# Performance work log

Hardware: AMD Instinct MI355X
Metric: run time of the kernel (lower is better)

The kernel has to match this reference:

```python
import jax, jax.numpy as jnp
import numpy as np

N, D, K = 16384, 256, 4096  # encoded vectors, embedding_dim, codebook_size


def setup_inputs() -> dict:
    key = jax.random.key(0)
    k_ze, k_cb = jax.random.split(key)
    ze = jax.random.normal(k_ze, (N, D), dtype=jnp.float32)
    codebook = jax.random.normal(k_cb, (K, D), dtype=jnp.float32)
    return {"ze": ze, "codebook": codebook}


def reference(ze, codebook):
    # Pairwise squared distances: ||ze||^2 + ||e||^2 - 2 ze e^T  -> [N, K]
    sq_norm = (
        jnp.sum(ze ** 2, axis=-1, keepdims=True)
        + jnp.sum(codebook ** 2, axis=1)
        - 2.0 * jnp.matmul(ze, codebook.T)
    )
    indices = jnp.argmin(sq_norm, axis=-1)            # [N]
    zq = jnp.take(codebook, indices, axis=0)          # [N, D] gather

    # VQ losses (stop-gradient mirrors .detach())
    vq_e_loss = jnp.mean((zq - jax.lax.stop_gradient(ze)) ** 2)
    vq_commit_loss = jnp.mean((jax.lax.stop_gradient(zq) - ze) ** 2)

    # perplexity: probs[i] = count_i / 10 (faithful to original, incl. /10)
    counts = jnp.zeros((K,), dtype=jnp.float32).at[indices].add(1.0)
    probs = counts / 10.0
    perplexity = jnp.exp(-jnp.sum(probs * jnp.log(probs + 1e-10)))

    return indices, zq, vq_e_loss, vq_commit_loss, perplexity
```

## Files before the change

kernel.cpp:

```cpp
#include <hip/hip_runtime.h>
#include <math.h>

#define N_TOT 16384
#define DIM   256
#define KCB   4096

typedef __attribute__((ext_vector_type(8)))  short s8v;
typedef __attribute__((ext_vector_type(16))) float f16v;

#define PK_OFF   32832
#define CBF_OFF  163904
#define WS_NEED  4358208ull
#define ZERO_W   36880

__device__ __forceinline__ void gload16(const void* g, void* l) {
  __builtin_amdgcn_global_load_lds(
      (const __attribute__((address_space(1))) unsigned int*)g,
      (__attribute__((address_space(3))) unsigned int*)l, 16, 0, 0);
}

__global__ __launch_bounds__(256)
void cb_prep_k(const float* __restrict__ cb, float* __restrict__ ws) {
  __shared__ float Cf[32 * 260];
  const int t = threadIdx.x, tile = blockIdx.x;
  for (int i = tile * 256 + t; i < ZERO_W; i += 128 * 256) ws[KCB + i] = 0.0f;

  const int c0 = tile * 32;
  {
    int r = t >> 3, q = t & 7;
    const float4* src4 = (const float4*)(cb + (size_t)(c0 + r) * DIM);
    float4* dst = (float4*)&Cf[r * 260];
    #pragma unroll
    for (int i = 0; i < 8; ++i) dst[q + 8 * i] = src4[q + 8 * i];
  }
  __syncthreads();

  const int col = t >> 3, j = t & 7;
  ushort* tb = (ushort*)((char*)ws + CBF_OFF) + (size_t)tile * 16384;
  const float* rowp = Cf + col * 260;
  float s = 0.0f;
  #pragma unroll
  for (int ks = 0; ks < 16; ++ks) {
    #pragma unroll
    for (int kh = 0; kh < 2; ++kh) {
      float x = rowp[ks * 16 + kh * 8 + j];
      s += x * x;
      unsigned xb = __float_as_uint(x);
      unsigned hb = xb & 0xFFFF0000u;
      float lf = x - __uint_as_float(hb);
      tb[ks * 512 + kh * 256 + t]        = (ushort)(xb >> 16);
      tb[8192 + ks * 512 + kh * 256 + t] = (ushort)(__float_as_uint(lf) >> 16);
    }
  }
  s += __shfl_down(s, 4, 8);
  s += __shfl_down(s, 2, 8);
  s += __shfl_down(s, 1, 8);
  if (j == 0) ws[c0 + col] = s;
}

__global__ __launch_bounds__(256, 2)
void vq_mfma_k(const float* __restrict__ ze, float* __restrict__ ws) {
  __shared__ __align__(16) char ldsU[66560];

  const int t    = threadIdx.x;
  const int lane = t & 63;
  const int w    = t >> 6;
  const int ln31 = lane & 31;
  const int hl   = lane >> 5;
  const int cq   = blockIdx.x >> 7;
  const int mb   = blockIdx.x & 127;
  const int m0   = mb * 128;

  const float* cbn = ws;
  unsigned long long* pk = (unsigned long long*)((char*)ws + PK_OFF);
  const char* cbF = (const char*)ws + CBF_OFF;

  s8v ah[16], al[16];
  float* Af = (float*)ldsU;
  #pragma unroll 1
  for (int ph = 0; ph < 2; ++ph) {
    __syncthreads();
    {
      int r = t >> 2, q = t & 3;
      const float4* src4 = (const float4*)(ze + (size_t)(m0 + ph * 64 + r) * DIM);
      float4* dst = (float4*)&Af[r * 260];
      #pragma unroll
      for (int i = 0; i < 16; ++i) dst[q + 4 * i] = src4[q + 4 * i];
    }
    __syncthreads();
    if ((w >> 1) == ph) {
      int rl = (w & 1) * 32 + ln31;
      const float* rowp = Af + rl * 260;
      #pragma unroll
      for (int ks = 0; ks < 16; ++ks) {
        float4 x0 = *(const float4*)(rowp + ks * 16 + hl * 8);
        float4 x1 = *(const float4*)(rowp + ks * 16 + hl * 8 + 4);
        float xs[8] = {x0.x, x0.y, x0.z, x0.w, x1.x, x1.y, x1.z, x1.w};
        #pragma unroll
        for (int j = 0; j < 8; ++j) {
          unsigned xb = __float_as_uint(xs[j]);
          unsigned hb = xb & 0xFFFF0000u;
          float lf = xs[j] - __uint_as_float(hb);
          ah[ks][j] = (short)(xb >> 16);
          al[ks][j] = (short)(__float_as_uint(lf) >> 16);
        }
      }
    }
  }
  __syncthreads();

  char* bufs0 = ldsU;
  char* bufs1 = ldsU + 32768;
  const char* qbase = cbF + (size_t)cq * 32 * 32768;

  {
    const char* g = qbase + (size_t)w * 1024 + (size_t)(lane & 63) * 16;
    char* lp = bufs0 + w * 1024 + (lane & 63) * 0;
    #pragma unroll
    for (int ii = 0; ii < 8; ++ii) gload16(g + ii * 4096, bufs0 + w * 1024 + ii * 4096);
    (void)lp;
  }

  float cvn = cbn[cq * 1024 + ln31];

  float best[16];
  int   bidx[16];
  #pragma unroll
  for (int r = 0; r < 16; ++r) { best[r] = -1e30f; bidx[r] = 0; }

  #pragma unroll 1
  for (int tt = 0; tt < 32; ++tt) {
    __syncthreads();
    if (tt + 1 < 32) {
      const char* g = qbase + (size_t)(tt + 1) * 32768 + (size_t)w * 1024 + (size_t)lane * 16;
      char* lp = ((tt + 1) & 1 ? bufs1 : bufs0) + w * 1024;
      #pragma unroll
      for (int ii = 0; ii < 8; ++ii) gload16(g + ii * 4096, lp + ii * 4096);
    }

    const float half_cv = 0.5f * cvn;
    if (tt + 1 < 32) cvn = cbn[cq * 1024 + (tt + 1) * 32 + ln31];
    const char* bc = (tt & 1) ? bufs1 : bufs0;

    f16v hh, xx;
    #pragma unroll
    for (int r = 0; r < 16; ++r) { hh[r] = 0.0f; xx[r] = 0.0f; }

    #pragma unroll
    for (int ks = 0; ks < 16; ++ks) {
      s8v bh = *(const s8v*)(bc + ks * 1024 + lane * 16);
      s8v bl = *(const s8v*)(bc + 16384 + ks * 1024 + lane * 16);
      hh = __builtin_amdgcn_mfma_f32_32x32x16_bf16(ah[ks], bh, hh, 0, 0, 0);
      xx = __builtin_amdgcn_mfma_f32_32x32x16_bf16(ah[ks], bl, xx, 0, 0, 0);
      xx = __builtin_amdgcn_mfma_f32_32x32x16_bf16(al[ks], bh, xx, 0, 0, 0);
    }

    const int c0 = cq * 1024 + tt * 32 + ln31;
    #pragma unroll
    for (int r = 0; r < 16; ++r) {
      float s = hh[r] + xx[r] - half_cv;
      if (s > best[r]) { best[r] = s; bidx[r] = c0; }
    }
  }

  #pragma unroll
  for (int r = 0; r < 16; ++r) {
    float s = best[r];
    int   c = bidx[r];
    #pragma unroll
    for (int mk = 1; mk < 32; mk <<= 1) {
      float os = __shfl_xor(s, mk, 64);
      int   oc = __shfl_xor(c, mk, 64);
      if (os > s || (os == s && oc < c)) { s = os; c = oc; }
    }
    if (ln31 == 0) {
      int row = m0 + w * 32 + (r & 3) + 8 * (r >> 2) + 4 * hl;
      unsigned u = __float_as_uint(s);
      unsigned enc = (u & 0x80000000u) ? ~u : (u | 0x80000000u);
      unsigned long long p = ((unsigned long long)enc << 32) | (unsigned)(KCB - 1 - c);
      atomicMax(&pk[row], p);
    }
  }
}

__global__ __launch_bounds__(256)
void gather_k(const float* __restrict__ ze, const float* __restrict__ cb,
              float* __restrict__ ws, float* __restrict__ out) {
  __shared__ int sIdx[32];
  const int t  = threadIdx.x;
  const int m0 = blockIdx.x * 32;
  float* counts   = ws + KCB;
  float* loss_sum = ws + 2 * KCB;
  const unsigned long long* pk = (const unsigned long long*)((const char*)ws + PK_OFF);

  if (t < 32) {
    unsigned long long p = pk[m0 + t];
    int col = KCB - 1 - (int)(unsigned)(p & 0xFFFFFFFFull);
    out[m0 + t] = (float)col;
    sIdx[t] = col;
    atomicAdd(&counts[col], 1.0f);
  }
  __syncthreads();

  float* out_zq = out + N_TOT;
  const int w = t >> 6, ln = t & 63;
  float lsum = 0.0f;
  #pragma unroll
  for (int p = 0; p < 8; ++p) {
    int r = w + 4 * p;
    float4 cvv = *(const float4*)(cb + (size_t)sIdx[r] * DIM + ln * 4);
    float4 zv  = *(const float4*)(ze + (size_t)(m0 + r) * DIM + ln * 4);
    *(float4*)(out_zq + (size_t)(m0 + r) * DIM + ln * 4) = cvv;
    float dx = cvv.x - zv.x, dy = cvv.y - zv.y, dz = cvv.z - zv.z, dw = cvv.w - zv.w;
    lsum += dx * dx + dy * dy + dz * dz + dw * dw;
  }
  #pragma unroll
  for (int off = 32; off > 0; off >>= 1) lsum += __shfl_down(lsum, off, 64);
  if (ln == 0) atomicAdd(loss_sum, lsum);
}

__global__ void zero_ws_k(float* __restrict__ ws, int nw) {
  int i = blockIdx.x * 256 + threadIdx.x;
  if (i < nw) ws[KCB + i] = 0.0f;
}

__global__ void cbnorm_k(const float* __restrict__ cb, float* __restrict__ ws) {
  int row  = blockIdx.x * 4 + (threadIdx.x >> 6);
  int lane = threadIdx.x & 63;
  float4 v = *(const float4*)(cb + (size_t)row * DIM + lane * 4);
  float s = v.x*v.x + v.y*v.y + v.z*v.z + v.w*v.w;
  #pragma unroll
  for (int off = 32; off > 0; off >>= 1) s += __shfl_down(s, off, 64);
  if (lane == 0) ws[row] = s;
}

#define FBM 32
#define FBN 64
#define FBD 128
__global__ __launch_bounds__(256, 4)
void vq_main_k(const float* __restrict__ ze, const float* __restrict__ cb,
               float* __restrict__ ws, float* __restrict__ out) {
  __shared__ float As[FBM * FBD];
  __shared__ float Bs[FBN * FBD];
  __shared__ float red_d[FBM * 16];
  __shared__ int   red_i[FBM * 16];
  __shared__ int   sIdx[FBM];

  const int t  = threadIdx.x;
  const int tx = t & 15;
  const int ty = t >> 4;
  const int m0 = blockIdx.x * FBM;

  const float* cbn = ws;
  float* counts    = ws + KCB;
  float* loss_sum  = ws + 2 * KCB;

  float best0 = 1e30f, best1 = 1e30f;
  int   bidx0 = 0,     bidx1 = 0;
  const int sA = ty & 7;
  const int sB = tx & 7;

  for (int kt = 0; kt < KCB / FBN; ++kt) {
    float cbnj[4];
    #pragma unroll
    for (int j = 0; j < 4; ++j) cbnj[j] = cbn[kt * FBN + tx + 16 * j];
    float acc[2][4];
    #pragma unroll
    for (int i = 0; i < 2; ++i)
      #pragma unroll
      for (int j = 0; j < 4; ++j) acc[i][j] = 0.0f;

    for (int dc = 0; dc < DIM / FBD; ++dc) {
      __syncthreads();
      {
        int c  = t & 31;
        int rb = t >> 5;
        #pragma unroll
        for (int p = 0; p < 4; ++p) {
          int r = rb + 8 * p;
          float4 v = *(const float4*)(ze + (size_t)(m0 + r) * DIM + dc * FBD + c * 4);
          *(float4*)&As[r * FBD + ((c ^ (r & 7)) << 2)] = v;
        }
        #pragma unroll
        for (int p = 0; p < 8; ++p) {
          int r = rb + 8 * p;
          float4 v = *(const float4*)(cb + (size_t)(kt * FBN + r) * DIM + dc * FBD + c * 4);
          *(float4*)&Bs[r * FBD + ((c ^ (r & 7)) << 2)] = v;
        }
      }
      __syncthreads();
      #pragma unroll 8
      for (int ds = 0; ds < FBD / 4; ++ds) {
        float4 a0 = *(const float4*)&As[ty * FBD + ((ds ^ sA) << 2)];
        float4 a1 = *(const float4*)&As[(ty + 16) * FBD + ((ds ^ sA) << 2)];
        float4 b[4];
        #pragma unroll
        for (int j = 0; j < 4; ++j)
          b[j] = *(const float4*)&Bs[(tx + 16 * j) * FBD + ((ds ^ sB) << 2)];
        #pragma unroll
        for (int j = 0; j < 4; ++j) {
          acc[0][j] = fmaf(a0.x, b[j].x, acc[0][j]);
          acc[0][j] = fmaf(a0.y, b[j].y, acc[0][j]);
          acc[0][j] = fmaf(a0.z, b[j].z, acc[0][j]);
          acc[0][j] = fmaf(a0.w, b[j].w, acc[0][j]);
          acc[1][j] = fmaf(a1.x, b[j].x, acc[1][j]);
          acc[1][j] = fmaf(a1.y, b[j].y, acc[1][j]);
          acc[1][j] = fmaf(a1.z, b[j].z, acc[1][j]);
          acc[1][j] = fmaf(a1.w, b[j].w, acc[1][j]);
        }
      }
    }
    #pragma unroll
    for (int j = 0; j < 4; ++j) {
      int kg = kt * FBN + tx + 16 * j;
      float d0 = cbnj[j] - 2.0f * acc[0][j];
      float d1 = cbnj[j] - 2.0f * acc[1][j];
      if (d0 < best0) { best0 = d0; bidx0 = kg; }
      if (d1 < best1) { best1 = d1; bidx1 = kg; }
    }
  }

  __syncthreads();
  red_d[ty * 16 + tx] = best0;        red_i[ty * 16 + tx] = bidx0;
  red_d[(ty + 16) * 16 + tx] = best1; red_i[(ty + 16) * 16 + tx] = bidx1;
  __syncthreads();

  if (t < FBM) {
    float bd = red_d[t * 16]; int bi = red_i[t * 16];
    #pragma unroll
    for (int q = 1; q < 16; ++q) {
      float d = red_d[t * 16 + q]; int i2 = red_i[t * 16 + q];
      if (d < bd || (d == bd && i2 < bi)) { bd = d; bi = i2; }
    }
    out[m0 + t] = (float)bi;
    sIdx[t] = bi;
    atomicAdd(&counts[bi], 1.0f);
  }
  __syncthreads();

  float* out_zq = out + N_TOT;
  const int wv = t >> 6, ln = t & 63;
  float lsum = 0.0f;
  #pragma unroll
  for (int p = 0; p < 8; ++p) {
    int r = wv + 4 * p;
    float4 cvv = *(const float4*)(cb + (size_t)sIdx[r] * DIM + ln * 4);
    float4 zv  = *(const float4*)(ze + (size_t)(m0 + r) * DIM + ln * 4);
    *(float4*)(out_zq + (size_t)(m0 + r) * DIM + ln * 4) = cvv;
    float dx = cvv.x - zv.x, dy = cvv.y - zv.y, dz = cvv.z - zv.z, dw = cvv.w - zv.w;
    lsum += dx*dx + dy*dy + dz*dz + dw*dw;
  }
  #pragma unroll
  for (int off = 32; off > 0; off >>= 1) lsum += __shfl_down(lsum, off, 64);
  if (ln == 0) atomicAdd(loss_sum, lsum);
}

__global__ void finalize_k(const float* __restrict__ ws, float* __restrict__ out) {
  __shared__ float red[256];
  int t = threadIdx.x;
  const float* counts = ws + KCB;
  float s = 0.0f;
  for (int k = t; k < KCB; k += 256) {
    float p = counts[k] * 0.1f;
    s += p * logf(p + 1e-10f);
  }
  red[t] = s;
  __syncthreads();
  for (int q = 128; q > 0; q >>= 1) { if (t < q) red[t] += red[t + q]; __syncthreads(); }
  if (t == 0) {
    float loss = ws[2 * KCB] / (float)((size_t)N_TOT * DIM);
    float* o = out + N_TOT + (size_t)N_TOT * DIM;
    o[0] = loss;
    o[1] = loss;
    o[2] = expf(-red[0]);
  }
}

extern "C" void kernel_launch(void* const* d_in, const int* in_sizes, int n_in,
                              void* d_out, int out_size, void* d_ws, size_t ws_size,
                              hipStream_t stream) {
  const float* ze = (const float*)d_in[0];
  const float* cb = (const float*)d_in[1];
  float* out = (float*)d_out;
  float* ws  = (float*)d_ws;

  if (ws_size >= WS_NEED) {
    cb_prep_k<<<128, 256, 0, stream>>>(cb, ws);
    vq_mfma_k<<<512, 256, 0, stream>>>(ze, ws);
    gather_k<<<N_TOT / 32, 256, 0, stream>>>(ze, cb, ws, out);
  } else {
    zero_ws_k<<<(KCB + 1 + 255) / 256, 256, 0, stream>>>(ws, KCB + 1);
    cbnorm_k<<<KCB / 4, 256, 0, stream>>>(cb, ws);
    vq_main_k<<<N_TOT / FBM, 256, 0, stream>>>(ze, cb, ws, out);
  }
  finalize_k<<<1, 256, 0, stream>>>(ws, out);
}
```

Before: 208.7 us.

## Fuse gather and finalize into MFMA distance kernel via last-block counters

Removes the separate gather and finalize launches. Each 128-row block tracks completion across its 4 codebook-quarter blocks with an atomic counter. The last quarter to finish does the argmin decode, zq gather, loss and count accumulation, and a global counter lets the very last block compute the perplexity and losses. This saves two kernel launches and their gaps, at the cost of threadfences, atomics, and serialized tail work in fewer blocks.

After: 225.4 us. +8.0%, slower.

```diff
diff --git a/kernel.cpp b/kernel.cpp
--- a/kernel.cpp
+++ b/kernel.cpp
@@ -8,10 +8,13 @@
 typedef __attribute__((ext_vector_type(8)))  short s8v;
 typedef __attribute__((ext_vector_type(16))) float f16v;
 
-#define PK_OFF   32832
-#define CBF_OFF  163904
-#define WS_NEED  4358208ull
-#define ZERO_W   36880
+#define LOSS_OFF  32768
+#define DONE_OFF  32772
+#define GDONE_OFF 33284
+#define PK_OFF    33344
+#define CBF_OFF   164416
+#define WS_NEED   4358720ull
+#define ZERO_W    37008
 
 __device__ __forceinline__ void gload16(const void* g, void* l) {
   __builtin_amdgcn_global_load_lds(
@@ -59,8 +62,10 @@
 }
 
 __global__ __launch_bounds__(256, 2)
-void vq_mfma_k(const float* __restrict__ ze, float* __restrict__ ws) {
+void vq_mfma_k(const float* __restrict__ ze, const float* __restrict__ cb,
+               float* __restrict__ ws, float* __restrict__ out) {
   __shared__ __align__(16) char ldsU[66560];
+  __shared__ int flagLast;
 
   const int t    = threadIdx.x;
   const int lane = t & 63;
@@ -114,11 +119,9 @@
   const char* qbase = cbF + (size_t)cq * 32 * 32768;
 
   {
-    const char* g = qbase + (size_t)w * 1024 + (size_t)(lane & 63) * 16;
-    char* lp = bufs0 + w * 1024 + (lane & 63) * 0;
+    const char* g = qbase + (size_t)w * 1024 + (size_t)lane * 16;
     #pragma unroll
     for (int ii = 0; ii < 8; ++ii) gload16(g + ii * 4096, bufs0 + w * 1024 + ii * 4096);
-    (void)lp;
   }
 
   float cvn = cbn[cq * 1024 + ln31];
@@ -181,20 +184,21 @@
       atomicMax(&pk[row], p);
     }
   }
-}
-
-__global__ __launch_bounds__(256)
-void gather_k(const float* __restrict__ ze, const float* __restrict__ cb,
-              float* __restrict__ ws, float* __restrict__ out) {
-  __shared__ int sIdx[32];
-  const int t  = threadIdx.x;
-  const int m0 = blockIdx.x * 32;
+
+  __threadfence();
+  unsigned* done  = (unsigned*)((char*)ws + DONE_OFF);
+  unsigned* gdone = (unsigned*)((char*)ws + GDONE_OFF);
+  if (t == 0) flagLast = (atomicAdd(&done[mb], 1u) == 3u) ? 1 : 0;
+  __syncthreads();
+  if (!flagLast) return;
+  __threadfence();
+
+  int*   sIdx     = (int*)ldsU;
   float* counts   = ws + KCB;
-  float* loss_sum = ws + 2 * KCB;
-  const unsigned long long* pk = (const unsigned long long*)((const char*)ws + PK_OFF);
-
-  if (t < 32) {
-    unsigned long long p = pk[m0 + t];
+  float* loss_sum = ws + LOSS_OFF / 4;
+
+  if (t < 128) {
+    unsigned long long p = atomicMax(&pk[m0 + t], 0ull);
     int col = KCB - 1 - (int)(unsigned)(p & 0xFFFFFFFFull);
     out[m0 + t] = (float)col;
     sIdx[t] = col;
@@ -203,20 +207,44 @@
   __syncthreads();
 
   float* out_zq = out + N_TOT;
-  const int w = t >> 6, ln = t & 63;
   float lsum = 0.0f;
-  #pragma unroll
-  for (int p = 0; p < 8; ++p) {
+  #pragma unroll 4
+  for (int p = 0; p < 32; ++p) {
     int r = w + 4 * p;
-    float4 cvv = *(const float4*)(cb + (size_t)sIdx[r] * DIM + ln * 4);
-    float4 zv  = *(const float4*)(ze + (size_t)(m0 + r) * DIM + ln * 4);
-    *(float4*)(out_zq + (size_t)(m0 + r) * DIM + ln * 4) = cvv;
+    float4 cvv = *(const float4*)(cb + (size_t)sIdx[r] * DIM + lane * 4);
+    float4 zv  = *(const float4*)(ze + (size_t)(m0 + r) * DIM + lane * 4);
+    *(float4*)(out_zq + (size_t)(m0 + r) * DIM + lane * 4) = cvv;
     float dx = cvv.x - zv.x, dy = cvv.y - zv.y, dz = cvv.z - zv.z, dw = cvv.w - zv.w;
     lsum += dx * dx + dy * dy + dz * dz + dw * dw;
   }
   #pragma unroll
   for (int off = 32; off > 0; off >>= 1) lsum += __shfl_down(lsum, off, 64);
-  if (ln == 0) atomicAdd(loss_sum, lsum);
+  if (lane == 0) atomicAdd(loss_sum, lsum);
+
+  __threadfence();
+  if (t == 0) flagLast = (atomicAdd(gdone, 1u) == 127u) ? 1 : 0;
+  __syncthreads();
+  if (!flagLast) return;
+  __threadfence();
+
+  float* red = (float*)(ldsU + 2048);
+  float s = 0.0f;
+  #pragma unroll
+  for (int k = t; k < KCB; k += 256) {
+    float c = atomicAdd(&counts[k], 0.0f);
+    float pr = c * 0.1f;
+    s += pr * logf(pr + 1e-10f);
+  }
+  red[t] = s;
+  __syncthreads();
+  for (int q = 128; q > 0; q >>= 1) { if (t < q) red[t] += red[t + q]; __syncthreads(); }
+  if (t == 0) {
+    float loss = atomicAdd(loss_sum, 0.0f) / (float)((size_t)N_TOT * DIM);
+    float* o = out + N_TOT + (size_t)N_TOT * DIM;
+    o[0] = loss;
+    o[1] = loss;
+    o[2] = expf(-red[0]);
+  }
 }
 
 __global__ void zero_ws_k(float* __restrict__ ws, int nw) {
@@ -386,12 +414,11 @@
 
   if (ws_size >= WS_NEED) {
     cb_prep_k<<<128, 256, 0, stream>>>(cb, ws);
-    vq_mfma_k<<<512, 256, 0, stream>>>(ze, ws);
-    gather_k<<<N_TOT / 32, 256, 0, stream>>>(ze, cb, ws, out);
+    vq_mfma_k<<<512, 256, 0, stream>>>(ze, cb, ws, out);
   } else {
     zero_ws_k<<<(KCB + 1 + 255) / 256, 256, 0, stream>>>(ws, KCB + 1);
     cbnorm_k<<<KCB / 4, 256, 0, stream>>>(cb, ws);
     vq_main_k<<<N_TOT / FBM, 256, 0, stream>>>(ze, cb, ws, out);
-  }
-  finalize_k<<<1, 256, 0, stream>>>(ws, out);
-}
+    finalize_k<<<1, 256, 0, stream>>>(ws, out);
+  }
+}
```
